# Kernel tuning notes

Measured on AMD Instinct MI355X. Metric: run time of the kernel, lower is better.

## Reference

```python
import jax, jax.numpy as jnp
import numpy as np

N_NODES = 100000
N_EDGES = 1600000
D_IN, D_H, D_OUT = 128, 128, 64


def gcn_conv(x, src, dst, W, b, n_nodes):
    """PyG GCNConv (eval): x' = D^{-1/2} (A+I) D^{-1/2} X W + b.
    src/dst already include self-loops."""
    h = x @ W  # [N, d_out] -- transform first (fewer FLOPs when d_out <= d_in)
    deg = jax.ops.segment_sum(jnp.ones_like(dst, dtype=h.dtype), dst, num_segments=n_nodes)
    dinv = jnp.where(deg > 0, jax.lax.rsqrt(deg), 0.0)
    norm = dinv[src] * dinv[dst]  # [E]
    msg = h[src] * norm[:, None]  # gather + scale
    out = jax.ops.segment_sum(msg, dst, num_segments=n_nodes)  # scatter-add
    return out + b


def setup_inputs() -> dict:
    key = jax.random.key(0)
    k = jax.random.split(key, 8)
    x = jax.random.normal(k[0], (N_NODES, D_IN), dtype=jnp.float32)
    edge_index = jax.random.randint(k[1], (2, N_EDGES), 0, N_NODES, dtype=jnp.int32)
    s = 0.1
    W1 = jax.random.normal(k[2], (D_IN, D_H), dtype=jnp.float32) * s
    b1 = jnp.zeros((D_H,), dtype=jnp.float32)
    W2 = jax.random.normal(k[3], (D_H, D_H), dtype=jnp.float32) * s
    b2 = jnp.zeros((D_H,), dtype=jnp.float32)
    W3 = jax.random.normal(k[4], (D_H, D_OUT), dtype=jnp.float32) * s
    b3 = jnp.zeros((D_OUT,), dtype=jnp.float32)
    return {"x": x, "edge_index": edge_index, "W1": W1, "b1": b1,
            "W2": W2, "b2": b2, "W3": W3, "b3": b3}


def reference(x, edge_index, W1, b1, W2, b2, W3, b3):
    n = x.shape[0]
    # add self-loops once (shared by all layers)
    loops = jnp.arange(n, dtype=edge_index.dtype)
    src = jnp.concatenate([edge_index[0], loops])
    dst = jnp.concatenate([edge_index[1], loops])
    h = gcn_conv(x, src, dst, W1, b1, n)
    h = jax.nn.relu(h)  # dropout = identity in eval mode
    h = gcn_conv(h, src, dst, W2, b2, n)
    h = jax.nn.relu(h)
    out = gcn_conv(h, src, dst, W3, b3, n)
    return out
```

## Files before the change

### kernel.cpp

```cpp
#include <hip/hip_runtime.h>
#include <hip/hip_fp16.h>

#define N_NODES 100000
#define N_EDGES 1600000
#define NBUCKET 196
#define CAP     8960
#define EPB     6250

typedef _Float16 half8 __attribute__((ext_vector_type(8)));
typedef float float4v __attribute__((ext_vector_type(4)));

__device__ __forceinline__ void fmix_lo(float& a, unsigned int w, float one) {
    asm("v_fma_mix_f32 %0, %1, %2, %0 op_sel:[0,0,0] op_sel_hi:[1,0,0]"
        : "+v"(a) : "v"(w), "v"(one));
}
__device__ __forceinline__ void fmix_hi(float& a, unsigned int w, float one) {
    asm("v_fma_mix_f32 %0, %1, %2, %0 op_sel:[1,0,0] op_sel_hi:[1,0,0]"
        : "+v"(a) : "v"(w), "v"(one));
}

__launch_bounds__(256)
__global__ void k_part_wswz(const int* __restrict__ src, const int* __restrict__ dst,
                            int* __restrict__ bcur, int* __restrict__ ebuf, int E,
                            const float* __restrict__ W1, const float* __restrict__ W2,
                            const float* __restrict__ W3, _Float16* __restrict__ wz1,
                            _Float16* __restrict__ wz2, _Float16* __restrict__ wz3) {
    if (blockIdx.x >= 256) {
        int t = (blockIdx.x - 256) * 256 + threadIdx.x;
        const float* W; _Float16* wsz; int BN;
        if (t < 2048)      { W = W1; wsz = wz1; BN = 128; }
        else if (t < 4096) { W = W2; wsz = wz2; BN = 128; t -= 2048; }
        else if (t < 5120) { W = W3; wsz = wz3; BN = 64;  t -= 4096; }
        else return;
        const int l = t & 63;
        const int kblk = (t >> 6) & 3;
        const int nt = t >> 8;
        const int krow = kblk * 32 + ((l >> 4) << 3);
        const int col = nt * 16 + (l & 15);
        _Float16 v[8];
#pragma unroll
        for (int j = 0; j < 8; ++j) v[j] = (_Float16)W[(krow + j) * BN + col];
        *(uint4*)&wsz[t << 3] = *(uint4*)v;
        return;
    }
    __shared__ int hist[200];
    __shared__ int basebkt[200];
    const int tid = threadIdx.x;
    if (tid < 200) hist[tid] = 0;
    __syncthreads();
    const int e0 = blockIdx.x * EPB, e1 = min(e0 + EPB, E);
    for (int e = e0 + tid; e < e1; e += 256) atomicAdd(&hist[dst[e] >> 9], 1);
    __syncthreads();
    if (tid < NBUCKET) {
        int h = hist[tid];
        basebkt[tid] = tid * CAP + (h ? atomicAdd(&bcur[tid], h) : 0);
    }
    __syncthreads();
    if (tid < 200) hist[tid] = 0;
    __syncthreads();
    for (int e = e0 + tid; e < e1; e += 256) {
        int d = dst[e];
        int bk = d >> 9;
        int o = atomicAdd(&hist[bk], 1);
        ebuf[basebkt[bk] + o] = (src[e] << 9) | (d & 511);
    }
}

__launch_bounds__(256)
__global__ void k_bsort(const int* __restrict__ ebuf, const int* __restrict__ bcur,
                        int* __restrict__ adj, int* __restrict__ stv,
                        int* __restrict__ deg, float* __restrict__ dinv, int N) {
    __shared__ int cnt[512];
    __shared__ int offs[512];
    const int b = blockIdx.x;
    const int tid = threadIdx.x;
    const int base = b * CAP;
    const int n_b = min(bcur[b], CAP);
    const int node0 = b << 9;
    cnt[tid] = 0; cnt[tid + 256] = 0;
    __syncthreads();
    for (int i = tid; i < n_b; i += 256)
        atomicAdd(&cnt[ebuf[base + i] & 511], 1);
    __syncthreads();
    if (tid < 64) {
        int v[8], tot = 0;
#pragma unroll
        for (int j = 0; j < 8; ++j) { int t = cnt[tid * 8 + j]; v[j] = tot; tot += t; }
        int inc = tot;
#pragma unroll
        for (int d = 1; d < 64; d <<= 1) {
            int u = __shfl_up(inc, d, 64);
            if (tid >= d) inc += u;
        }
        const int excl = inc - tot;
#pragma unroll
        for (int j = 0; j < 8; ++j) offs[tid * 8 + j] = excl + v[j];
    }
    __syncthreads();
#pragma unroll
    for (int h = 0; h < 2; ++h) {
        int local = tid + h * 256;
        int node = node0 + local;
        if (node < N) {
            stv[node] = base + offs[local];
            deg[node] = cnt[local];
            dinv[node] = rsqrtf((float)(cnt[local] + 1));
        }
    }
    __syncthreads();
    for (int i = tid; i < n_b; i += 256) {
        int pk = ebuf[base + i];
        int pos = atomicAdd(&offs[pk & 511], 1);
        adj[base + pos] = pk >> 9;
    }
}

template <int BN, bool AFP16>
__launch_bounds__(256, 4)
__global__ void k_gemm_mfma(const void* __restrict__ Xv, const _Float16* __restrict__ wsz,
                            const float* __restrict__ dinv, __half* __restrict__ out, int N) {
    constexpr int NT = BN / 16;
    constexpr int PAD = 8;
    __shared__ __align__(16) _Float16 smem[BN * 128];

    const int tid = threadIdx.x;
    for (int i = tid; i < BN * 16; i += 256)
        *(uint4*)&smem[i << 3] = *(const uint4*)&wsz[i << 3];

    const int w = tid >> 6;
    const int lane = tid & 63;
    const int q = lane >> 4;
    const int m = lane & 15;
    const int row0 = blockIdx.x * 64;
    const int arow = row0 + w * 16 + m;
    const int arowc = arow < N ? arow : N - 1;

    float4v acc[NT];
#pragma unroll
    for (int nt = 0; nt < NT; ++nt) acc[nt] = (float4v){0.f, 0.f, 0.f, 0.f};

    __syncthreads();

#pragma unroll
    for (int kblk = 0; kblk < 4; ++kblk) {
        half8 af;
        if constexpr (AFP16) {
            const _Float16* A = (const _Float16*)Xv + (size_t)arowc * 128 + (q << 3);
            af = *(const half8*)(A + kblk * 32);
        } else {
            const float* A = (const float*)Xv + (size_t)arowc * 128 + (q << 3);
            float4 a0 = *(const float4*)(A + kblk * 32);
            float4 a1 = *(const float4*)(A + kblk * 32 + 4);
            af[0] = (_Float16)a0.x; af[1] = (_Float16)a0.y;
            af[2] = (_Float16)a0.z; af[3] = (_Float16)a0.w;
            af[4] = (_Float16)a1.x; af[5] = (_Float16)a1.y;
            af[6] = (_Float16)a1.z; af[7] = (_Float16)a1.w;
        }
#pragma unroll
        for (int nt = 0; nt < NT; ++nt) {
            half8 bf = *(const half8*)&smem[(((nt << 2) + kblk) << 9) + (lane << 3)];
            acc[nt] = __builtin_amdgcn_mfma_f32_16x16x32_f16(af, bf, acc[nt], 0, 0, 0);
        }
    }

    float s[4];
#pragma unroll
    for (int r = 0; r < 4; ++r) {
        int rr = row0 + w * 16 + q * 4 + r;
        s[r] = dinv[rr < N ? rr : N - 1];
    }
    __syncthreads();
    _Float16* eb = smem;
#pragma unroll
    for (int nt = 0; nt < NT; ++nt)
#pragma unroll
        for (int r = 0; r < 4; ++r)
            eb[(w * 16 + q * 4 + r) * (BN + PAD) + nt * 16 + m] = (_Float16)(acc[nt][r] * s[r]);
    __syncthreads();
    constexpr int CPR = BN / 8;
    for (int i = tid; i < 64 * CPR; i += 256) {
        int row = i / CPR;
        int cf = (i % CPR) * 8;
        if (row0 + row < N)
            *(uint4*)&out[(size_t)(row0 + row) * BN + cf] = *(uint4*)&eb[row * (BN + PAD) + cf];
    }
}

template <bool RELU>
__launch_bounds__(256)
__global__ void k_agg128(const __half* __restrict__ tp, const int* __restrict__ adj,
                         const int* __restrict__ startv, const int* __restrict__ deg,
                         const float* __restrict__ dinv, const float* __restrict__ bias,
                         _Float16* __restrict__ out, int N) {
    const int n0 = (blockIdx.x << 3) + ((threadIdx.x >> 6) << 1);
    const int lane = threadIdx.x & 63;
    if (n0 >= N) return;
    const bool has1 = (n0 + 1) < N;
    const int n1 = has1 ? n0 + 1 : n0;
    const int s0 = startv[n0], s1 = startv[n1];
    const int c0 = deg[n0];
    const int c1 = has1 ? deg[n1] : 0;
    const float one = 1.0f;
    const int g = lane >> 4;
    const int sl = lane & 15;
    const uint4* rowb = (const uint4*)tp;

    float a0[8] = {0.f, 0.f, 0.f, 0.f, 0.f, 0.f, 0.f, 0.f};
    float a1[8] = {0.f, 0.f, 0.f, 0.f, 0.f, 0.f, 0.f, 0.f};
    auto addrow = [&](float* acc, uint4 v) {
        fmix_lo(acc[0], v.x, one); fmix_hi(acc[1], v.x, one);
        fmix_lo(acc[2], v.y, one); fmix_hi(acc[3], v.y, one);
        fmix_lo(acc[4], v.z, one); fmix_hi(acc[5], v.z, one);
        fmix_lo(acc[6], v.w, one); fmix_hi(acc[7], v.w, one);
    };

    {
        uint4 r0 = rowb[(size_t)n0 * 16 + sl];
        uint4 r1 = rowb[(size_t)n1 * 16 + sl];
        if (g == 0) { addrow(a0, r0); if (has1) addrow(a1, r1); }
    }

    int e = 0;
    const int mc = min(c0, c1);
    for (; e + 16 <= mc; e += 16) {
        int j0[4], j1[4];
#pragma unroll
        for (int u = 0; u < 4; ++u) { j0[u] = adj[s0 + e + 4 * u + g]; j1[u] = adj[s1 + e + 4 * u + g]; }
        uint4 v0[4], v1[4];
#pragma unroll
        for (int u = 0; u < 4; ++u) { v0[u] = rowb[(size_t)j0[u] * 16 + sl]; v1[u] = rowb[(size_t)j1[u] * 16 + sl]; }
#pragma unroll
        for (int u = 0; u < 4; ++u) { addrow(a0, v0[u]); addrow(a1, v1[u]); }
    }

    auto finish = [&](float* acc, int s, int cnt, int eS) {
        int ee = eS;
        for (; ee + 16 <= cnt; ee += 16) {
            int j[4];
#pragma unroll
            for (int u = 0; u < 4; ++u) j[u] = adj[s + ee + 4 * u + g];
            uint4 v[4];
#pragma unroll
            for (int u = 0; u < 4; ++u) v[u] = rowb[(size_t)j[u] * 16 + sl];
#pragma unroll
            for (int u = 0; u < 4; ++u) addrow(acc, v[u]);
        }
        if (ee + 8 <= cnt) {
            int j[2];
#pragma unroll
            for (int u = 0; u < 2; ++u) j[u] = adj[s + ee + 4 * u + g];
            uint4 v[2];
#pragma unroll
            for (int u = 0; u < 2; ++u) v[u] = rowb[(size_t)j[u] * 16 + sl];
#pragma unroll
            for (int u = 0; u < 2; ++u) addrow(acc, v[u]);
            ee += 8;
        }
        if (ee + 4 <= cnt) {
            addrow(acc, rowb[(size_t)adj[s + ee + g] * 16 + sl]);
            ee += 4;
        }
        if (ee + g < cnt)
            addrow(acc, rowb[(size_t)adj[s + ee + g] * 16 + sl]);
    };
    finish(a0, s0, c0, e);
    if (has1) finish(a1, s1, c1, e);

#pragma unroll
    for (int i = 0; i < 8; ++i) {
        a0[i] += __shfl_xor(a0[i], 32);
        a0[i] += __shfl_xor(a0[i], 16);
        a1[i] += __shfl_xor(a1[i], 32);
        a1[i] += __shfl_xor(a1[i], 16);
    }
    if (g == 0) {
        float4 b0 = *(const float4*)&bias[sl * 8];
        float4 b1 = *(const float4*)&bias[sl * 8 + 4];
        const float di0 = dinv[n0];
        float o[8];
        o[0] = di0 * a0[0] + b0.x; o[1] = di0 * a0[1] + b0.y;
        o[2] = di0 * a0[2] + b0.z; o[3] = di0 * a0[3] + b0.w;
        o[4] = di0 * a0[4] + b1.x; o[5] = di0 * a0[5] + b1.y;
        o[6] = di0 * a0[6] + b1.z; o[7] = di0 * a0[7] + b1.w;
        if (RELU)
#pragma unroll
            for (int i = 0; i < 8; ++i) o[i] = fmaxf(o[i], 0.f);
        __half2 ov[4];
#pragma unroll
        for (int i = 0; i < 4; ++i) ov[i] = __floats2half2_rn(o[2 * i], o[2 * i + 1]);
        *(uint4*)&out[(size_t)n0 * 128 + sl * 8] = *(uint4*)ov;
        if (has1) {
            const float di1 = dinv[n1];
            o[0] = di1 * a1[0] + b0.x; o[1] = di1 * a1[1] + b0.y;
            o[2] = di1 * a1[2] + b0.z; o[3] = di1 * a1[3] + b0.w;
            o[4] = di1 * a1[4] + b1.x; o[5] = di1 * a1[5] + b1.y;
            o[6] = di1 * a1[6] + b1.z; o[7] = di1 * a1[7] + b1.w;
            if (RELU)
#pragma unroll
                for (int i = 0; i < 8; ++i) o[i] = fmaxf(o[i], 0.f);
#pragma unroll
            for (int i = 0; i < 4; ++i) ov[i] = __floats2half2_rn(o[2 * i], o[2 * i + 1]);
            *(uint4*)&out[(size_t)n1 * 128 + sl * 8] = *(uint4*)ov;
        }
    }
}

__launch_bounds__(256)
__global__ void k_agg64(const __half* __restrict__ tp, const int* __restrict__ adj,
                        const int* __restrict__ startv, const int* __restrict__ deg,
                        const float* __restrict__ dinv, const float* __restrict__ bias,
                        float* __restrict__ out, int N) {
    const int n0 = (blockIdx.x << 3) + ((threadIdx.x >> 6) << 1);
    const int lane = threadIdx.x & 63;
    if (n0 >= N) return;
    const bool has1 = (n0 + 1) < N;
    const int n1 = has1 ? n0 + 1 : n0;
    const int s0 = startv[n0], s1 = startv[n1];
    const int c0 = deg[n0];
    const int c1 = has1 ? deg[n1] : 0;
    const float one = 1.0f;
    const int g = lane >> 4;
    const int sl = lane & 15;
    const uint2* rowb = (const uint2*)tp;

    float a0[4] = {0.f, 0.f, 0.f, 0.f};
    float a1[4] = {0.f, 0.f, 0.f, 0.f};
    auto addrow = [&](float* acc, uint2 v) {
        fmix_lo(acc[0], v.x, one); fmix_hi(acc[1], v.x, one);
        fmix_lo(acc[2], v.y, one); fmix_hi(acc[3], v.y, one);
    };
    {
        uint2 r0 = rowb[(size_t)n0 * 16 + sl];
        uint2 r1 = rowb[(size_t)n1 * 16 + sl];
        if (g == 0) { addrow(a0, r0); if (has1) addrow(a1, r1); }
    }

    int e = 0;
    const int mc = min(c0, c1);
    for (; e + 16 <= mc; e += 16) {
        int j0[4], j1[4];
#pragma unroll
        for (int u = 0; u < 4; ++u) { j0[u] = adj[s0 + e + 4 * u + g]; j1[u] = adj[s1 + e + 4 * u + g]; }
        uint2 v0[4], v1[4];
#pragma unroll
        for (int u = 0; u < 4; ++u) { v0[u] = rowb[(size_t)j0[u] * 16 + sl]; v1[u] = rowb[(size_t)j1[u] * 16 + sl]; }
#pragma unroll
        for (int u = 0; u < 4; ++u) { addrow(a0, v0[u]); addrow(a1, v1[u]); }
    }

    auto finish = [&](float* acc, int s, int cnt, int eS) {
        int ee = eS;
        for (; ee + 16 <= cnt; ee += 16) {
            int j[4];
#pragma unroll
            for (int u = 0; u < 4; ++u) j[u] = adj[s + ee + 4 * u + g];
            uint2 v[4];
#pragma unroll
            for (int u = 0; u < 4; ++u) v[u] = rowb[(size_t)j[u] * 16 + sl];
#pragma unroll
            for (int u = 0; u < 4; ++u) addrow(acc, v[u]);
        }
        if (ee + 8 <= cnt) {
            int j[2];
#pragma unroll
            for (int u = 0; u < 2; ++u) j[u] = adj[s + ee + 4 * u + g];
            uint2 v[2];
#pragma unroll
            for (int u = 0; u < 2; ++u) v[u] = rowb[(size_t)j[u] * 16 + sl];
#pragma unroll
            for (int u = 0; u < 2; ++u) addrow(acc, v[u]);
            ee += 8;
        }
        if (ee + 4 <= cnt) {
            addrow(acc, rowb[(size_t)adj[s + ee + g] * 16 + sl]);
            ee += 4;
        }
        if (ee + g < cnt)
            addrow(acc, rowb[(size_t)adj[s + ee + g] * 16 + sl]);
    };
    finish(a0, s0, c0, e);
    if (has1) finish(a1, s1, c1, e);

#pragma unroll
    for (int i = 0; i < 4; ++i) {
        a0[i] += __shfl_xor(a0[i], 32);
        a0[i] += __shfl_xor(a0[i], 16);
        a1[i] += __shfl_xor(a1[i], 32);
        a1[i] += __shfl_xor(a1[i], 16);
    }
    if (g == 0) {
        float4 bb = *(const float4*)&bias[sl * 4];
        const float di0 = dinv[n0];
        float4 o;
        o.x = di0 * a0[0] + bb.x; o.y = di0 * a0[1] + bb.y;
        o.z = di0 * a0[2] + bb.z; o.w = di0 * a0[3] + bb.w;
        *(float4*)&out[(size_t)n0 * 64 + sl * 4] = o;
        if (has1) {
            const float di1 = dinv[n1];
            o.x = di1 * a1[0] + bb.x; o.y = di1 * a1[1] + bb.y;
            o.z = di1 * a1[2] + bb.z; o.w = di1 * a1[3] + bb.w;
            *(float4*)&out[(size_t)n1 * 64 + sl * 4] = o;
        }
    }
}

extern "C" void kernel_launch(void* const* d_in, const int* in_sizes, int n_in,
                              void* d_out, int out_size, void* d_ws, size_t ws_size,
                              hipStream_t stream) {
    const float* x  = (const float*)d_in[0];
    const int*   ei = (const int*)d_in[1];
    const float* W1 = (const float*)d_in[2];
    const float* b1 = (const float*)d_in[3];
    const float* W2 = (const float*)d_in[4];
    const float* b2 = (const float*)d_in[5];
    const float* W3 = (const float*)d_in[6];
    const float* b3 = (const float*)d_in[7];
    float* out = (float*)d_out;
    const int* src = ei;
    const int* dst = ei + N_EDGES;

    char* p = (char*)d_ws;
    __half* tp      = (__half*)p;    p += (size_t)N_NODES * 128 * 2;
    _Float16* hbuf  = (_Float16*)p;  p += (size_t)N_NODES * 128 * 2;
    int*   deg  = (int*)p;    p += (size_t)N_NODES * 4;
    float* dinv = (float*)p;  p += (size_t)N_NODES * 4;
    int*   stv  = (int*)p;    p += (size_t)N_NODES * 4;
    int*   bCur = (int*)p;    p += 1024;
    int*   adj  = (int*)p;    p += (size_t)NBUCKET * CAP * 4 + 16384;
    _Float16* wz1 = (_Float16*)p; p += 16384 * 2;
    _Float16* wz2 = (_Float16*)p; p += 16384 * 2;
    _Float16* wz3 = (_Float16*)p; p += 8192 * 2;
    size_t need = (size_t)(p - (char*)d_ws);
    if (ws_size < need) return;

    int* ebuf = (int*)tp;

    hipMemsetAsync(bCur, 0, 1024, stream);
    k_part_wswz<<<276, 256, 0, stream>>>(src, dst, bCur, ebuf, N_EDGES,
                                         W1, W2, W3, wz1, wz2, wz3);
    k_bsort<<<NBUCKET, 256, 0, stream>>>(ebuf, bCur, adj, stv, deg, dinv, N_NODES);

    const int gb = (N_NODES + 63) / 64;
    const int ab = (N_NODES + 7) / 8;
    k_gemm_mfma<128, false><<<gb, 256, 0, stream>>>(x, wz1, dinv, tp, N_NODES);
    k_agg128<true><<<ab, 256, 0, stream>>>(tp, adj, stv, deg, dinv, b1, hbuf, N_NODES);
    k_gemm_mfma<128, true><<<gb, 256, 0, stream>>>(hbuf, wz2, dinv, tp, N_NODES);
    k_agg128<true><<<ab, 256, 0, stream>>>(tp, adj, stv, deg, dinv, b2, hbuf, N_NODES);
    k_gemm_mfma<64, true><<<gb, 256, 0, stream>>>(hbuf, wz3, dinv, tp, N_NODES);
    k_agg64<<<ab, 256, 0, stream>>>(tp, adj, stv, deg, dinv, b3, out, N_NODES);
}
```

Measured before the change: 356.4 us.

## Split aggregation feature columns across XCDs so each XCD caches one slice

```diff
diff --git a/kernel.cpp b/kernel.cpp
--- a/kernel.cpp
+++ b/kernel.cpp
@@ -192,7 +192,11 @@
                          const int* __restrict__ startv, const int* __restrict__ deg,
                          const float* __restrict__ dinv, const float* __restrict__ bias,
                          _Float16* __restrict__ out, int N) {
-    const int n0 = (blockIdx.x << 3) + ((threadIdx.x >> 6) << 1);
+    const int b = blockIdx.x;
+    const int xcd = b & 7;
+    const int sc = xcd >> 1;
+    const int bis = ((b >> 3) << 1) | (xcd & 1);
+    const int n0 = (bis << 3) + ((threadIdx.x >> 6) << 1);
     const int lane = threadIdx.x & 63;
     if (n0 >= N) return;
     const bool has1 = (n0 + 1) < N;
@@ -203,20 +207,18 @@
     const float one = 1.0f;
     const int g = lane >> 4;
     const int sl = lane & 15;
-    const uint4* rowb = (const uint4*)tp;
-
-    float a0[8] = {0.f, 0.f, 0.f, 0.f, 0.f, 0.f, 0.f, 0.f};
-    float a1[8] = {0.f, 0.f, 0.f, 0.f, 0.f, 0.f, 0.f, 0.f};
-    auto addrow = [&](float* acc, uint4 v) {
-        fmix_lo(acc[0], v.x, one); fmix_hi(acc[1], v.x, one);
-        fmix_lo(acc[2], v.y, one); fmix_hi(acc[3], v.y, one);
-        fmix_lo(acc[4], v.z, one); fmix_hi(acc[5], v.z, one);
-        fmix_lo(acc[6], v.w, one); fmix_hi(acc[7], v.w, one);
+    const unsigned* rowu = (const unsigned*)tp;
+    const int co = sc * 16 + sl;
+
+    float a0[2] = {0.f, 0.f};
+    float a1[2] = {0.f, 0.f};
+    auto addrow = [&](float* acc, unsigned v) {
+        fmix_lo(acc[0], v, one); fmix_hi(acc[1], v, one);
     };
 
     {
-        uint4 r0 = rowb[(size_t)n0 * 16 + sl];
-        uint4 r1 = rowb[(size_t)n1 * 16 + sl];
+        unsigned r0 = rowu[(size_t)n0 * 64 + co];
+        unsigned r1 = rowu[(size_t)n1 * 64 + co];
         if (g == 0) { addrow(a0, r0); if (has1) addrow(a1, r1); }
     }
 
@@ -226,9 +228,9 @@
         int j0[4], j1[4];
 #pragma unroll
         for (int u = 0; u < 4; ++u) { j0[u] = adj[s0 + e + 4 * u + g]; j1[u] = adj[s1 + e + 4 * u + g]; }
-        uint4 v0[4], v1[4];
-#pragma unroll
-        for (int u = 0; u < 4; ++u) { v0[u] = rowb[(size_t)j0[u] * 16 + sl]; v1[u] = rowb[(size_t)j1[u] * 16 + sl]; }
+        unsigned v0[4], v1[4];
+#pragma unroll
+        for (int u = 0; u < 4; ++u) { v0[u] = rowu[(size_t)j0[u] * 64 + co]; v1[u] = rowu[(size_t)j1[u] * 64 + co]; }
 #pragma unroll
         for (int u = 0; u < 4; ++u) { addrow(a0, v0[u]); addrow(a1, v1[u]); }
     }
@@ -239,9 +241,9 @@
             int j[4];
 #pragma unroll
             for (int u = 0; u < 4; ++u) j[u] = adj[s + ee + 4 * u + g];
-            uint4 v[4];
-#pragma unroll
-            for (int u = 0; u < 4; ++u) v[u] = rowb[(size_t)j[u] * 16 + sl];
+            unsigned v[4];
+#pragma unroll
+            for (int u = 0; u < 4; ++u) v[u] = rowu[(size_t)j[u] * 64 + co];
 #pragma unroll
             for (int u = 0; u < 4; ++u) addrow(acc, v[u]);
         }
@@ -249,58 +251,44 @@
             int j[2];
 #pragma unroll
             for (int u = 0; u < 2; ++u) j[u] = adj[s + ee + 4 * u + g];
-            uint4 v[2];
-#pragma unroll
-            for (int u = 0; u < 2; ++u) v[u] = rowb[(size_t)j[u] * 16 + sl];
+            unsigned v[2];
+#pragma unroll
+            for (int u = 0; u < 2; ++u) v[u] = rowu[(size_t)j[u] * 64 + co];
 #pragma unroll
             for (int u = 0; u < 2; ++u) addrow(acc, v[u]);
             ee += 8;
         }
         if (ee + 4 <= cnt) {
-            addrow(acc, rowb[(size_t)adj[s + ee + g] * 16 + sl]);
+            addrow(acc, rowu[(size_t)adj[s + ee + g] * 64 + co]);
             ee += 4;
         }
         if (ee + g < cnt)
-            addrow(acc, rowb[(size_t)adj[s + ee + g] * 16 + sl]);
+            addrow(acc, rowu[(size_t)adj[s + ee + g] * 64 + co]);
     };
     finish(a0, s0, c0, e);
     if (has1) finish(a1, s1, c1, e);
 
 #pragma unroll
-    for (int i = 0; i < 8; ++i) {
+    for (int i = 0; i < 2; ++i) {
         a0[i] += __shfl_xor(a0[i], 32);
         a0[i] += __shfl_xor(a0[i], 16);
         a1[i] += __shfl_xor(a1[i], 32);
         a1[i] += __shfl_xor(a1[i], 16);
     }
     if (g == 0) {
-        float4 b0 = *(const float4*)&bias[sl * 8];
-        float4 b1 = *(const float4*)&bias[sl * 8 + 4];
+        const float bx = bias[sc * 32 + sl * 2];
+        const float by = bias[sc * 32 + sl * 2 + 1];
         const float di0 = dinv[n0];
-        float o[8];
-        o[0] = di0 * a0[0] + b0.x; o[1] = di0 * a0[1] + b0.y;
-        o[2] = di0 * a0[2] + b0.z; o[3] = di0 * a0[3] + b0.w;
-        o[4] = di0 * a0[4] + b1.x; o[5] = di0 * a0[5] + b1.y;
-        o[6] = di0 * a0[6] + b1.z; o[7] = di0 * a0[7] + b1.w;
-        if (RELU)
-#pragma unroll
-            for (int i = 0; i < 8; ++i) o[i] = fmaxf(o[i], 0.f);
-        __half2 ov[4];
-#pragma unroll
-        for (int i = 0; i < 4; ++i) ov[i] = __floats2half2_rn(o[2 * i], o[2 * i + 1]);
-        *(uint4*)&out[(size_t)n0 * 128 + sl * 8] = *(uint4*)ov;
+        float ox = di0 * a0[0] + bx, oy = di0 * a0[1] + by;
+        if (RELU) { ox = fmaxf(ox, 0.f); oy = fmaxf(oy, 0.f); }
+        __half2 ov = __floats2half2_rn(ox, oy);
+        *(unsigned*)&out[(size_t)n0 * 128 + sc * 32 + sl * 2] = *(unsigned*)&ov;
         if (has1) {
             const float di1 = dinv[n1];
-            o[0] = di1 * a1[0] + b0.x; o[1] = di1 * a1[1] + b0.y;
-            o[2] = di1 * a1[2] + b0.z; o[3] = di1 * a1[3] + b0.w;
-            o[4] = di1 * a1[4] + b1.x; o[5] = di1 * a1[5] + b1.y;
-            o[6] = di1 * a1[6] + b1.z; o[7] = di1 * a1[7] + b1.w;
-            if (RELU)
-#pragma unroll
-                for (int i = 0; i < 8; ++i) o[i] = fmaxf(o[i], 0.f);
-#pragma unroll
-            for (int i = 0; i < 4; ++i) ov[i] = __floats2half2_rn(o[2 * i], o[2 * i + 1]);
-            *(uint4*)&out[(size_t)n1 * 128 + sl * 8] = *(uint4*)ov;
+            ox = di1 * a1[0] + bx; oy = di1 * a1[1] + by;
+            if (RELU) { ox = fmaxf(ox, 0.f); oy = fmaxf(oy, 0.f); }
+            ov = __floats2half2_rn(ox, oy);
+            *(unsigned*)&out[(size_t)n1 * 128 + sc * 32 + sl * 2] = *(unsigned*)&ov;
         }
     }
 }
@@ -310,7 +298,11 @@
                         const int* __restrict__ startv, const int* __restrict__ deg,
                         const float* __restrict__ dinv, const float* __restrict__ bias,
                         float* __restrict__ out, int N) {
-    const int n0 = (blockIdx.x << 3) + ((threadIdx.x >> 6) << 1);
+    const int b = blockIdx.x;
+    const int xcd = b & 7;
+    const int sc = xcd >> 2;
+    const int bis = ((b >> 3) << 2) | (xcd & 3);
+    const int n0 = (bis << 3) + ((threadIdx.x >> 6) << 1);
     const int lane = threadIdx.x & 63;
     if (n0 >= N) return;
     const bool has1 = (n0 + 1) < N;
@@ -321,17 +313,17 @@
     const float one = 1.0f;
     const int g = lane >> 4;
     const int sl = lane & 15;
-    const uint2* rowb = (const uint2*)tp;
-
-    float a0[4] = {0.f, 0.f, 0.f, 0.f};
-    float a1[4] = {0.f, 0.f, 0.f, 0.f};
-    auto addrow = [&](float* acc, uint2 v) {
-        fmix_lo(acc[0], v.x, one); fmix_hi(acc[1], v.x, one);
-        fmix_lo(acc[2], v.y, one); fmix_hi(acc[3], v.y, one);
+    const unsigned* rowu = (const unsigned*)tp;
+    const int co = sc * 16 + sl;
+
+    float a0[2] = {0.f, 0.f};
+    float a1[2] = {0.f, 0.f};
+    auto addrow = [&](float* acc, unsigned v) {
+        fmix_lo(acc[0], v, one); fmix_hi(acc[1], v, one);
     };
     {
-        uint2 r0 = rowb[(size_t)n0 * 16 + sl];
-        uint2 r1 = rowb[(size_t)n1 * 16 + sl];
+        unsigned r0 = rowu[(size_t)n0 * 32 + co];
+        unsigned r1 = rowu[(size_t)n1 * 32 + co];
         if (g == 0) { addrow(a0, r0); if (has1) addrow(a1, r1); }
     }
 
@@ -341,9 +333,9 @@
         int j0[4], j1[4];
 #pragma unroll
         for (int u = 0; u < 4; ++u) { j0[u] = adj[s0 + e + 4 * u + g]; j1[u] = adj[s1 + e + 4 * u + g]; }
-        uint2 v0[4], v1[4];
-#pragma unroll
-        for (int u = 0; u < 4; ++u) { v0[u] = rowb[(size_t)j0[u] * 16 + sl]; v1[u] = rowb[(size_t)j1[u] * 16 + sl]; }
+        unsigned v0[4], v1[4];
+#pragma unroll
+        for (int u = 0; u < 4; ++u) { v0[u] = rowu[(size_t)j0[u] * 32 + co]; v1[u] = rowu[(size_t)j1[u] * 32 + co]; }
 #pragma unroll
         for (int u = 0; u < 4; ++u) { addrow(a0, v0[u]); addrow(a1, v1[u]); }
     }
@@ -354,9 +346,9 @@
             int j[4];
 #pragma unroll
             for (int u = 0; u < 4; ++u) j[u] = adj[s + ee + 4 * u + g];
-            uint2 v[4];
-#pragma unroll
-            for (int u = 0; u < 4; ++u) v[u] = rowb[(size_t)j[u] * 16 + sl];
+            unsigned v[4];
+#pragma unroll
+            for (int u = 0; u < 4; ++u) v[u] = rowu[(size_t)j[u] * 32 + co];
 #pragma unroll
             for (int u = 0; u < 4; ++u) addrow(acc, v[u]);
         }
@@ -364,42 +356,41 @@
             int j[2];
 #pragma unroll
             for (int u = 0; u < 2; ++u) j[u] = adj[s + ee + 4 * u + g];
-            uint2 v[2];
-#pragma unroll
-            for (int u = 0; u < 2; ++u) v[u] = rowb[(size_t)j[u] * 16 + sl];
+            unsigned v[2];
+#pragma unroll
+            for (int u = 0; u < 2; ++u) v[u] = rowu[(size_t)j[u] * 32 + co];
 #pragma unroll
             for (int u = 0; u < 2; ++u) addrow(acc, v[u]);
             ee += 8;
         }
         if (ee + 4 <= cnt) {
-            addrow(acc, rowb[(size_t)adj[s + ee + g] * 16 + sl]);
+            addrow(acc, rowu[(size_t)adj[s + ee + g] * 32 + co]);
             ee += 4;
         }
         if (ee + g < cnt)
-            addrow(acc, rowb[(size_t)adj[s + ee + g] * 16 + sl]);
+            addrow(acc, rowu[(size_t)adj[s + ee + g] * 32 + co]);
     };
     finish(a0, s0, c0, e);
     if (has1) finish(a1, s1, c1, e);
 
 #pragma unroll
-    for (int i = 0; i < 4; ++i) {
+    for (int i = 0; i < 2; ++i) {
         a0[i] += __shfl_xor(a0[i], 32);
         a0[i] += __shfl_xor(a0[i], 16);
         a1[i] += __shfl_xor(a1[i], 32);
         a1[i] += __shfl_xor(a1[i], 16);
     }
     if (g == 0) {
-        float4 bb = *(const float4*)&bias[sl * 4];
+        const float bx = bias[sc * 32 + sl * 2];
+        const float by = bias[sc * 32 + sl * 2 + 1];
         const float di0 = dinv[n0];
-        float4 o;
-        o.x = di0 * a0[0] + bb.x; o.y = di0 * a0[1] + bb.y;
-        o.z = di0 * a0[2] + bb.z; o.w = di0 * a0[3] + bb.w;
-        *(float4*)&out[(size_t)n0 * 64 + sl * 4] = o;
+        float2 o;
+        o.x = di0 * a0[0] + bx; o.y = di0 * a0[1] + by;
+        *(float2*)&out[(size_t)n0 * 64 + sc * 32 + sl * 2] = o;
         if (has1) {
             const float di1 = dinv[n1];
-            o.x = di1 * a1[0] + bb.x; o.y = di1 * a1[1] + bb.y;
-            o.z = di1 * a1[2] + bb.z; o.w = di1 * a1[3] + bb.w;
-            *(float4*)&out[(size_t)n1 * 64 + sl * 4] = o;
+            o.x = di1 * a1[0] + bx; o.y = di1 * a1[1] + by;
+            *(float2*)&out[(size_t)n1 * 64 + sc * 32 + sl * 2] = o;
         }
     }
 }
@@ -441,11 +432,12 @@
     k_bsort<<<NBUCKET, 256, 0, stream>>>(ebuf, bCur, adj, stv, deg, dinv, N_NODES);
 
     const int gb = (N_NODES + 63) / 64;
-    const int ab = (N_NODES + 7) / 8;
+    const int ab128 = 12500 * 4;
+    const int ab64  = 12500 * 2;
     k_gemm_mfma<128, false><<<gb, 256, 0, stream>>>(x, wz1, dinv, tp, N_NODES);
-    k_agg128<true><<<ab, 256, 0, stream>>>(tp, adj, stv, deg, dinv, b1, hbuf, N_NODES);
+    k_agg128<true><<<ab128, 256, 0, stream>>>(tp, adj, stv, deg, dinv, b1, hbuf, N_NODES);
     k_gemm_mfma<128, true><<<gb, 256, 0, stream>>>(hbuf, wz2, dinv, tp, N_NODES);
-    k_agg128<true><<<ab, 256, 0, stream>>>(tp, adj, stv, deg, dinv, b2, hbuf, N_NODES);
+    k_agg128<true><<<ab128, 256, 0, stream>>>(tp, adj, stv, deg, dinv, b2, hbuf, N_NODES);
     k_gemm_mfma<64, true><<<gb, 256, 0, stream>>>(hbuf, wz3, dinv, tp, N_NODES);
-    k_agg64<<<ab, 256, 0, stream>>>(tp, adj, stv, deg, dinv, b3, out, N_NODES);
-}
+    k_agg64<<<ab64, 256, 0, stream>>>(tp, adj, stv, deg, dinv, b3, out, N_NODES);
+}
```

Result: slower. 531.3 us (+49.1%).

## Fuse all GCN stages into one persistent cooperative kernel with grid syncs

Applied to the files above, without the earlier changes.

```diff
diff --git a/kernel.cpp b/kernel.cpp
--- a/kernel.cpp
+++ b/kernel.cpp
@@ -1,11 +1,16 @@
 #include <hip/hip_runtime.h>
 #include <hip/hip_fp16.h>
+#include <hip/hip_cooperative_groups.h>
+
+namespace cg = cooperative_groups;
 
 #define N_NODES 100000
 #define N_EDGES 1600000
 #define NBUCKET 196
 #define CAP     8960
 #define EPB     6250
+#define VB_GEMM ((N_NODES + 63) / 64)
+#define VB_AGG  ((N_NODES + 7) / 8)
 
 typedef _Float16 half8 __attribute__((ext_vector_type(8)));
 typedef float float4v __attribute__((ext_vector_type(4)));
@@ -19,36 +24,33 @@
         : "+v"(a) : "v"(w), "v"(one));
 }
 
-__launch_bounds__(256)
-__global__ void k_part_wswz(const int* __restrict__ src, const int* __restrict__ dst,
-                            int* __restrict__ bcur, int* __restrict__ ebuf, int E,
-                            const float* __restrict__ W1, const float* __restrict__ W2,
-                            const float* __restrict__ W3, _Float16* __restrict__ wz1,
-                            _Float16* __restrict__ wz2, _Float16* __restrict__ wz3) {
-    if (blockIdx.x >= 256) {
-        int t = (blockIdx.x - 256) * 256 + threadIdx.x;
-        const float* W; _Float16* wsz; int BN;
-        if (t < 2048)      { W = W1; wsz = wz1; BN = 128; }
-        else if (t < 4096) { W = W2; wsz = wz2; BN = 128; t -= 2048; }
-        else if (t < 5120) { W = W3; wsz = wz3; BN = 64;  t -= 4096; }
-        else return;
-        const int l = t & 63;
-        const int kblk = (t >> 6) & 3;
-        const int nt = t >> 8;
-        const int krow = kblk * 32 + ((l >> 4) << 3);
-        const int col = nt * 16 + (l & 15);
-        _Float16 v[8];
-#pragma unroll
-        for (int j = 0; j < 8; ++j) v[j] = (_Float16)W[(krow + j) * BN + col];
-        *(uint4*)&wsz[t << 3] = *(uint4*)v;
-        return;
-    }
-    __shared__ int hist[200];
-    __shared__ int basebkt[200];
-    const int tid = threadIdx.x;
+
+__device__ __forceinline__ void wswz_one(int t, const float* __restrict__ W1,
+                                         const float* __restrict__ W2, const float* __restrict__ W3,
+                                         _Float16* __restrict__ wz1, _Float16* __restrict__ wz2,
+                                         _Float16* __restrict__ wz3) {
+    const float* W; _Float16* wsz; int BN;
+    if (t < 2048)      { W = W1; wsz = wz1; BN = 128; }
+    else if (t < 4096) { W = W2; wsz = wz2; BN = 128; t -= 2048; }
+    else               { W = W3; wsz = wz3; BN = 64;  t -= 4096; }
+    const int l = t & 63;
+    const int kblk = (t >> 6) & 3;
+    const int nt = t >> 8;
+    const int krow = kblk * 32 + ((l >> 4) << 3);
+    const int col = nt * 16 + (l & 15);
+    _Float16 v[8];
+#pragma unroll
+    for (int j = 0; j < 8; ++j) v[j] = (_Float16)W[(krow + j) * BN + col];
+    *(uint4*)&wsz[t << 3] = *(uint4*)v;
+}
+
+__device__ __forceinline__ void d_part(int vb, int tid, int* hist, int* basebkt,
+                                       const int* __restrict__ src, const int* __restrict__ dst,
+                                       int* __restrict__ bcur, int* __restrict__ ebuf, int E) {
+    __syncthreads();
     if (tid < 200) hist[tid] = 0;
     __syncthreads();
-    const int e0 = blockIdx.x * EPB, e1 = min(e0 + EPB, E);
+    const int e0 = vb * EPB, e1 = min(e0 + EPB, E);
     for (int e = e0 + tid; e < e1; e += 256) atomicAdd(&hist[dst[e] >> 9], 1);
     __syncthreads();
     if (tid < NBUCKET) {
@@ -66,17 +68,14 @@
     }
 }
 
-__launch_bounds__(256)
-__global__ void k_bsort(const int* __restrict__ ebuf, const int* __restrict__ bcur,
-                        int* __restrict__ adj, int* __restrict__ stv,
-                        int* __restrict__ deg, float* __restrict__ dinv, int N) {
-    __shared__ int cnt[512];
-    __shared__ int offs[512];
-    const int b = blockIdx.x;
-    const int tid = threadIdx.x;
-    const int base = b * CAP;
-    const int n_b = min(bcur[b], CAP);
-    const int node0 = b << 9;
+__device__ __forceinline__ void d_bsort(int vb, int tid, int* cnt, int* offs,
+                                        const int* __restrict__ ebuf, const int* __restrict__ bcur,
+                                        int* __restrict__ adj, int* __restrict__ stv,
+                                        int* __restrict__ deg, float* __restrict__ dinv, int N) {
+    __syncthreads();
+    const int base = vb * CAP;
+    const int n_b = min(bcur[vb], CAP);
+    const int node0 = vb << 9;
     cnt[tid] = 0; cnt[tid + 256] = 0;
     __syncthreads();
     for (int i = tid; i < n_b; i += 256)
@@ -116,14 +115,12 @@
 }
 
 template <int BN, bool AFP16>
-__launch_bounds__(256, 4)
-__global__ void k_gemm_mfma(const void* __restrict__ Xv, const _Float16* __restrict__ wsz,
-                            const float* __restrict__ dinv, __half* __restrict__ out, int N) {
+__device__ __forceinline__ void d_gemm(int vb, int tid, _Float16* smem,
+                                       const void* __restrict__ Xv, const _Float16* __restrict__ wsz,
+                                       const float* __restrict__ dinv, __half* __restrict__ out, int N) {
     constexpr int NT = BN / 16;
     constexpr int PAD = 8;
-    __shared__ __align__(16) _Float16 smem[BN * 128];
-
-    const int tid = threadIdx.x;
+    __syncthreads();
     for (int i = tid; i < BN * 16; i += 256)
         *(uint4*)&smem[i << 3] = *(const uint4*)&wsz[i << 3];
 
@@ -131,7 +128,7 @@
     const int lane = tid & 63;
     const int q = lane >> 4;
     const int m = lane & 15;
-    const int row0 = blockIdx.x * 64;
+    const int row0 = vb * 64;
     const int arow = row0 + w * 16 + m;
     const int arowc = arow < N ? arow : N - 1;
 
@@ -187,13 +184,13 @@
 }
 
 template <bool RELU>
-__launch_bounds__(256)
-__global__ void k_agg128(const __half* __restrict__ tp, const int* __restrict__ adj,
-                         const int* __restrict__ startv, const int* __restrict__ deg,
-                         const float* __restrict__ dinv, const float* __restrict__ bias,
-                         _Float16* __restrict__ out, int N) {
-    const int n0 = (blockIdx.x << 3) + ((threadIdx.x >> 6) << 1);
-    const int lane = threadIdx.x & 63;
+__device__ __forceinline__ void d_agg128(int vb, int tid,
+                                         const __half* __restrict__ tp, const int* __restrict__ adj,
+                                         const int* __restrict__ startv, const int* __restrict__ deg,
+                                         const float* __restrict__ dinv, const float* __restrict__ bias,
+                                         _Float16* __restrict__ out, int N) {
+    const int n0 = (vb << 3) + ((tid >> 6) << 1);
+    const int lane = tid & 63;
     if (n0 >= N) return;
     const bool has1 = (n0 + 1) < N;
     const int n1 = has1 ? n0 + 1 : n0;
@@ -305,13 +302,13 @@
     }
 }
 
-__launch_bounds__(256)
-__global__ void k_agg64(const __half* __restrict__ tp, const int* __restrict__ adj,
-                        const int* __restrict__ startv, const int* __restrict__ deg,
-                        const float* __restrict__ dinv, const float* __restrict__ bias,
-                        float* __restrict__ out, int N) {
-    const int n0 = (blockIdx.x << 3) + ((threadIdx.x >> 6) << 1);
-    const int lane = threadIdx.x & 63;
+__device__ __forceinline__ void d_agg64(int vb, int tid,
+                                        const __half* __restrict__ tp, const int* __restrict__ adj,
+                                        const int* __restrict__ startv, const int* __restrict__ deg,
+                                        const float* __restrict__ dinv, const float* __restrict__ bias,
+                                        float* __restrict__ out, int N) {
+    const int n0 = (vb << 3) + ((tid >> 6) << 1);
+    const int lane = tid & 63;
     if (n0 >= N) return;
     const bool has1 = (n0 + 1) < N;
     const int n1 = has1 ? n0 + 1 : n0;
@@ -402,6 +399,100 @@
             *(float4*)&out[(size_t)n1 * 64 + sl * 4] = o;
         }
     }
+}
+
+__global__ void __launch_bounds__(256, 4)
+k_mega(const float* x, const int* src, const int* dst,
+       const float* W1, const float* W2, const float* W3,
+       const float* b1, const float* b2, const float* b3,
+       float* out, __half* tp, _Float16* hbuf,
+       int* deg, float* dinv, int* stv, int* bcur, int* adj,
+       _Float16* wz1, _Float16* wz2, _Float16* wz3) {
+    __shared__ __align__(16) _Float16 smem[128 * 128];
+    int* ilds = (int*)smem;
+    cg::grid_group gg = cg::this_grid();
+    const int tid = threadIdx.x;
+    const int nb = gridDim.x;
+    int* ebuf = (int*)tp;
+
+    {
+        const int gid = blockIdx.x * 256 + tid;
+        for (int t = gid; t < 5120; t += nb * 256)
+            wswz_one(t, W1, W2, W3, wz1, wz2, wz3);
+        for (int i = gid; i < 256; i += nb * 256) bcur[i] = 0;
+    }
+    gg.sync();
+    for (int vb = blockIdx.x; vb < 256; vb += nb)
+        d_part(vb, tid, ilds, ilds + 200, src, dst, bcur, ebuf, N_EDGES);
+    gg.sync();
+    for (int vb = blockIdx.x; vb < NBUCKET; vb += nb)
+        d_bsort(vb, tid, ilds, ilds + 512, ebuf, bcur, adj, stv, deg, dinv, N_NODES);
+    gg.sync();
+    for (int vb = blockIdx.x; vb < VB_GEMM; vb += nb)
+        d_gemm<128, false>(vb, tid, smem, x, wz1, dinv, tp, N_NODES);
+    gg.sync();
+    for (int vb = blockIdx.x; vb < VB_AGG; vb += nb)
+        d_agg128<true>(vb, tid, tp, adj, stv, deg, dinv, b1, hbuf, N_NODES);
+    gg.sync();
+    for (int vb = blockIdx.x; vb < VB_GEMM; vb += nb)
+        d_gemm<128, true>(vb, tid, smem, hbuf, wz2, dinv, tp, N_NODES);
+    gg.sync();
+    for (int vb = blockIdx.x; vb < VB_AGG; vb += nb)
+        d_agg128<true>(vb, tid, tp, adj, stv, deg, dinv, b2, hbuf, N_NODES);
+    gg.sync();
+    for (int vb = blockIdx.x; vb < VB_GEMM; vb += nb)
+        d_gemm<64, true>(vb, tid, smem, hbuf, wz3, dinv, tp, N_NODES);
+    gg.sync();
+    for (int vb = blockIdx.x; vb < VB_AGG; vb += nb)
+        d_agg64(vb, tid, (const __half*)tp, adj, stv, deg, dinv, b3, out, N_NODES);
+}
+
+__launch_bounds__(256)
+__global__ void k_part_wswz(const int* __restrict__ src, const int* __restrict__ dst,
+                            int* __restrict__ bcur, int* __restrict__ ebuf, int E,
+                            const float* __restrict__ W1, const float* __restrict__ W2,
+                            const float* __restrict__ W3, _Float16* __restrict__ wz1,
+                            _Float16* __restrict__ wz2, _Float16* __restrict__ wz3) {
+    __shared__ int hb[400];
+    if (blockIdx.x >= 256) {
+        int t = (blockIdx.x - 256) * 256 + threadIdx.x;
+        if (t < 5120) wswz_one(t, W1, W2, W3, wz1, wz2, wz3);
+        return;
+    }
+    d_part(blockIdx.x, threadIdx.x, hb, hb + 200, src, dst, bcur, ebuf, E);
+}
+
+__launch_bounds__(256)
+__global__ void k_bsort(const int* __restrict__ ebuf, const int* __restrict__ bcur,
+                        int* __restrict__ adj, int* __restrict__ stv,
+                        int* __restrict__ deg, float* __restrict__ dinv, int N) {
+    __shared__ int cb[1024];
+    d_bsort(blockIdx.x, threadIdx.x, cb, cb + 512, ebuf, bcur, adj, stv, deg, dinv, N);
+}
+
+template <int BN, bool AFP16>
+__launch_bounds__(256, 4)
+__global__ void k_gemm_mfma(const void* __restrict__ Xv, const _Float16* __restrict__ wsz,
+                            const float* __restrict__ dinv, __half* __restrict__ out, int N) {
+    __shared__ __align__(16) _Float16 smem[BN * 128];
+    d_gemm<BN, AFP16>(blockIdx.x, threadIdx.x, smem, Xv, wsz, dinv, out, N);
+}
+
+template <bool RELU>
+__launch_bounds__(256)
+__global__ void k_agg128(const __half* __restrict__ tp, const int* __restrict__ adj,
+                         const int* __restrict__ startv, const int* __restrict__ deg,
+                         const float* __restrict__ dinv, const float* __restrict__ bias,
+                         _Float16* __restrict__ out, int N) {
+    d_agg128<RELU>(blockIdx.x, threadIdx.x, tp, adj, startv, deg, dinv, bias, out, N);
+}
+
+__launch_bounds__(256)
+__global__ void k_agg64(const __half* __restrict__ tp, const int* __restrict__ adj,
+                        const int* __restrict__ startv, const int* __restrict__ deg,
+                        const float* __restrict__ dinv, const float* __restrict__ bias,
+                        float* __restrict__ out, int N) {
+    d_agg64(blockIdx.x, threadIdx.x, tp, adj, startv, deg, dinv, bias, out, N);
 }
 
 extern "C" void kernel_launch(void* const* d_in, const int* in_sizes, int n_in,
@@ -435,13 +526,30 @@
 
     int* ebuf = (int*)tp;
 
+    int maxb = 0;
+    hipError_t oe = hipOccupancyMaxActiveBlocksPerMultiprocessor(&maxb, k_mega, 256, 0);
+    int nblocks = (oe == hipSuccess && maxb > 0) ? min(1024, maxb * 256) : 0;
+    hipError_t cerr = hipErrorUnknown;
+    if (nblocks > 0) {
+        void* kargs[] = {(void*)&x, (void*)&src, (void*)&dst,
+                         (void*)&W1, (void*)&W2, (void*)&W3,
+                         (void*)&b1, (void*)&b2, (void*)&b3,
+                         (void*)&out, (void*)&tp, (void*)&hbuf,
+                         (void*)&deg, (void*)&dinv, (void*)&stv,
+                         (void*)&bCur, (void*)&adj,
+                         (void*)&wz1, (void*)&wz2, (void*)&wz3};
+        cerr = hipLaunchCooperativeKernel((const void*)k_mega, dim3(nblocks), dim3(256),
+                                          kargs, 0, stream);
+    }
+    if (cerr == hipSuccess) return;
+
     hipMemsetAsync(bCur, 0, 1024, stream);
     k_part_wswz<<<276, 256, 0, stream>>>(src, dst, bCur, ebuf, N_EDGES,
                                          W1, W2, W3, wz1, wz2, wz3);
     k_bsort<<<NBUCKET, 256, 0, stream>>>(ebuf, bCur, adj, stv, deg, dinv, N_NODES);
 
-    const int gb = (N_NODES + 63) / 64;
-    const int ab = (N_NODES + 7) / 8;
+    const int gb = VB_GEMM;
+    const int ab = VB_AGG;
     k_gemm_mfma<128, false><<<gb, 256, 0, stream>>>(x, wz1, dinv, tp, N_NODES);
     k_agg128<true><<<ab, 256, 0, stream>>>(tp, adj, stv, deg, dinv, b1, hbuf, N_NODES);
     k_gemm_mfma<128, true><<<gb, 256, 0, stream>>>(hbuf, wz2, dinv, tp, N_NODES);
```

Result: slower. 1.014 ms (+184.5%).

## Fuse aggregation with next layer's GEMM via shared-memory MFMA tile

Applied to the files above, without the earlier changes.

```diff
diff --git a/kernel.cpp b/kernel.cpp
--- a/kernel.cpp
+++ b/kernel.cpp
@@ -186,20 +186,25 @@
     }
 }
 
-template <bool RELU>
-__launch_bounds__(256)
-__global__ void k_agg128(const __half* __restrict__ tp, const int* __restrict__ adj,
+template <int BN>
+__launch_bounds__(512)
+__global__ void k_aggemm(const __half* __restrict__ tp, const int* __restrict__ adj,
                          const int* __restrict__ startv, const int* __restrict__ deg,
                          const float* __restrict__ dinv, const float* __restrict__ bias,
-                         _Float16* __restrict__ out, int N) {
-    const int n0 = (blockIdx.x << 3) + ((threadIdx.x >> 6) << 1);
-    const int lane = threadIdx.x & 63;
-    if (n0 >= N) return;
-    const bool has1 = (n0 + 1) < N;
-    const int n1 = has1 ? n0 + 1 : n0;
-    const int s0 = startv[n0], s1 = startv[n1];
-    const int c0 = deg[n0];
-    const int c1 = has1 ? deg[n1] : 0;
+                         const _Float16* __restrict__ wsz, __half* __restrict__ outtp, int N) {
+    __shared__ __align__(16) _Float16 hl[16][136];
+    const int tid = threadIdx.x;
+    const int w = tid >> 6;
+    const int lane = tid & 63;
+    const int blk0 = blockIdx.x << 4;
+    const int n0 = blk0 + (w << 1);
+    const bool v0 = n0 < N;
+    const bool v1 = (n0 + 1) < N;
+    const int nn0 = v0 ? n0 : 0;
+    const int nn1 = v1 ? n0 + 1 : nn0;
+    const int s0 = v0 ? startv[nn0] : 0, s1 = v1 ? startv[nn1] : 0;
+    const int c0 = v0 ? deg[nn0] : 0;
+    const int c1 = v1 ? deg[nn1] : 0;
     const float one = 1.0f;
     const int g = lane >> 4;
     const int sl = lane & 15;
@@ -214,10 +219,10 @@
         fmix_lo(acc[6], v.w, one); fmix_hi(acc[7], v.w, one);
     };
 
-    {
-        uint4 r0 = rowb[(size_t)n0 * 16 + sl];
-        uint4 r1 = rowb[(size_t)n1 * 16 + sl];
-        if (g == 0) { addrow(a0, r0); if (has1) addrow(a1, r1); }
+    if (v0) {
+        uint4 r0 = rowb[(size_t)nn0 * 16 + sl];
+        uint4 r1 = rowb[(size_t)nn1 * 16 + sl];
+        if (g == 0) { addrow(a0, r0); if (v1) addrow(a1, r1); }
     }
 
     int e = 0;
@@ -226,11 +231,11 @@
         int j0[4], j1[4];
 #pragma unroll
         for (int u = 0; u < 4; ++u) { j0[u] = adj[s0 + e + 4 * u + g]; j1[u] = adj[s1 + e + 4 * u + g]; }
-        uint4 v0[4], v1[4];
-#pragma unroll
-        for (int u = 0; u < 4; ++u) { v0[u] = rowb[(size_t)j0[u] * 16 + sl]; v1[u] = rowb[(size_t)j1[u] * 16 + sl]; }
-#pragma unroll
-        for (int u = 0; u < 4; ++u) { addrow(a0, v0[u]); addrow(a1, v1[u]); }
+        uint4 v0v[4], v1v[4];
+#pragma unroll
+        for (int u = 0; u < 4; ++u) { v0v[u] = rowb[(size_t)j0[u] * 16 + sl]; v1v[u] = rowb[(size_t)j1[u] * 16 + sl]; }
+#pragma unroll
+        for (int u = 0; u < 4; ++u) { addrow(a0, v0v[u]); addrow(a1, v1v[u]); }
     }
 
     auto finish = [&](float* acc, int s, int cnt, int eS) {
@@ -264,7 +269,7 @@
             addrow(acc, rowb[(size_t)adj[s + ee + g] * 16 + sl]);
     };
     finish(a0, s0, c0, e);
-    if (has1) finish(a1, s1, c1, e);
+    if (v1) finish(a1, s1, c1, e);
 
 #pragma unroll
     for (int i = 0; i < 8; ++i) {
@@ -273,34 +278,48 @@
         a1[i] += __shfl_xor(a1[i], 32);
         a1[i] += __shfl_xor(a1[i], 16);
     }
-    if (g == 0) {
+    if (g == 0 && v0) {
         float4 b0 = *(const float4*)&bias[sl * 8];
         float4 b1 = *(const float4*)&bias[sl * 8 + 4];
-        const float di0 = dinv[n0];
+        const float di0 = dinv[nn0];
         float o[8];
-        o[0] = di0 * a0[0] + b0.x; o[1] = di0 * a0[1] + b0.y;
-        o[2] = di0 * a0[2] + b0.z; o[3] = di0 * a0[3] + b0.w;
-        o[4] = di0 * a0[4] + b1.x; o[5] = di0 * a0[5] + b1.y;
-        o[6] = di0 * a0[6] + b1.z; o[7] = di0 * a0[7] + b1.w;
-        if (RELU)
-#pragma unroll
-            for (int i = 0; i < 8; ++i) o[i] = fmaxf(o[i], 0.f);
+        o[0] = fmaxf(di0 * a0[0] + b0.x, 0.f); o[1] = fmaxf(di0 * a0[1] + b0.y, 0.f);
+        o[2] = fmaxf(di0 * a0[2] + b0.z, 0.f); o[3] = fmaxf(di0 * a0[3] + b0.w, 0.f);
+        o[4] = fmaxf(di0 * a0[4] + b1.x, 0.f); o[5] = fmaxf(di0 * a0[5] + b1.y, 0.f);
+        o[6] = fmaxf(di0 * a0[6] + b1.z, 0.f); o[7] = fmaxf(di0 * a0[7] + b1.w, 0.f);
         __half2 ov[4];
 #pragma unroll
         for (int i = 0; i < 4; ++i) ov[i] = __floats2half2_rn(o[2 * i], o[2 * i + 1]);
-        *(uint4*)&out[(size_t)n0 * 128 + sl * 8] = *(uint4*)ov;
-        if (has1) {
-            const float di1 = dinv[n1];
-            o[0] = di1 * a1[0] + b0.x; o[1] = di1 * a1[1] + b0.y;
-            o[2] = di1 * a1[2] + b0.z; o[3] = di1 * a1[3] + b0.w;
-            o[4] = di1 * a1[4] + b1.x; o[5] = di1 * a1[5] + b1.y;
-            o[6] = di1 * a1[6] + b1.z; o[7] = di1 * a1[7] + b1.w;
-            if (RELU)
-#pragma unroll
-                for (int i = 0; i < 8; ++i) o[i] = fmaxf(o[i], 0.f);
+        *(uint4*)&hl[w * 2][sl * 8] = *(uint4*)ov;
+        if (v1) {
+            const float di1 = dinv[nn1];
+            o[0] = fmaxf(di1 * a1[0] + b0.x, 0.f); o[1] = fmaxf(di1 * a1[1] + b0.y, 0.f);
+            o[2] = fmaxf(di1 * a1[2] + b0.z, 0.f); o[3] = fmaxf(di1 * a1[3] + b0.w, 0.f);
+            o[4] = fmaxf(di1 * a1[4] + b1.x, 0.f); o[5] = fmaxf(di1 * a1[5] + b1.y, 0.f);
+            o[6] = fmaxf(di1 * a1[6] + b1.z, 0.f); o[7] = fmaxf(di1 * a1[7] + b1.w, 0.f);
 #pragma unroll
             for (int i = 0; i < 4; ++i) ov[i] = __floats2half2_rn(o[2 * i], o[2 * i + 1]);
-            *(uint4*)&out[(size_t)n1 * 128 + sl * 8] = *(uint4*)ov;
+            *(uint4*)&hl[w * 2 + 1][sl * 8] = *(uint4*)ov;
+        }
+    }
+    __syncthreads();
+
+    if (w < BN / 16) {
+        const int q = lane >> 4;
+        const int m = lane & 15;
+        float4v acc = (float4v){0.f, 0.f, 0.f, 0.f};
+#pragma unroll
+        for (int kblk = 0; kblk < 4; ++kblk) {
+            half8 af = *(const half8*)&hl[m][(q << 3) + kblk * 32];
+            half8 bf = *(const half8*)&wsz[(((w << 2) + kblk) << 9) + (lane << 3)];
+            acc = __builtin_amdgcn_mfma_f32_16x16x32_f16(af, bf, acc, 0, 0, 0);
+        }
+#pragma unroll
+        for (int r = 0; r < 4; ++r) {
+            const int row = q * 4 + r;
+            const int node = blk0 + row;
+            if (node < N)
+                outtp[(size_t)node * BN + w * 16 + m] = __float2half(acc[r] * dinv[node]);
         }
     }
 }
@@ -420,8 +439,8 @@
     const int* dst = ei + N_EDGES;
 
     char* p = (char*)d_ws;
-    __half* tp      = (__half*)p;    p += (size_t)N_NODES * 128 * 2;
-    _Float16* hbuf  = (_Float16*)p;  p += (size_t)N_NODES * 128 * 2;
+    __half* tpA     = (__half*)p;    p += (size_t)N_NODES * 128 * 2;
+    __half* tpB     = (__half*)p;    p += (size_t)N_NODES * 128 * 2;
     int*   deg  = (int*)p;    p += (size_t)N_NODES * 4;
     float* dinv = (float*)p;  p += (size_t)N_NODES * 4;
     int*   stv  = (int*)p;    p += (size_t)N_NODES * 4;
@@ -433,7 +452,7 @@
     size_t need = (size_t)(p - (char*)d_ws);
     if (ws_size < need) return;
 
-    int* ebuf = (int*)tp;
+    int* ebuf = (int*)tpA;
 
     hipMemsetAsync(bCur, 0, 1024, stream);
     k_part_wswz<<<276, 256, 0, stream>>>(src, dst, bCur, ebuf, N_EDGES,
@@ -441,11 +460,10 @@
     k_bsort<<<NBUCKET, 256, 0, stream>>>(ebuf, bCur, adj, stv, deg, dinv, N_NODES);
 
     const int gb = (N_NODES + 63) / 64;
+    const int fb = (N_NODES + 15) / 16;
     const int ab = (N_NODES + 7) / 8;
-    k_gemm_mfma<128, false><<<gb, 256, 0, stream>>>(x, wz1, dinv, tp, N_NODES);
-    k_agg128<true><<<ab, 256, 0, stream>>>(tp, adj, stv, deg, dinv, b1, hbuf, N_NODES);
-    k_gemm_mfma<128, true><<<gb, 256, 0, stream>>>(hbuf, wz2, dinv, tp, N_NODES);
-    k_agg128<true><<<ab, 256, 0, stream>>>(tp, adj, stv, deg, dinv, b2, hbuf, N_NODES);
-    k_gemm_mfma<64, true><<<gb, 256, 0, stream>>>(hbuf, wz3, dinv, tp, N_NODES);
-    k_agg64<<<ab, 256, 0, stream>>>(tp, adj, stv, deg, dinv, b3, out, N_NODES);
-}
+    k_gemm_mfma<128, false><<<gb, 256, 0, stream>>>(x, wz1, dinv, tpA, N_NODES);
+    k_aggemm<128><<<fb, 512, 0, stream>>>(tpA, adj, stv, deg, dinv, b1, wz2, tpB, N_NODES);
+    k_aggemm<64><<<fb, 512, 0, stream>>>(tpB, adj, stv, deg, dinv, b2, wz3, tpA, N_NODES);
+    k_agg64<<<ab, 256, 0, stream>>>(tpA, adj, stv, deg, dinv, b3, out, N_NODES);
+}
```

After: 354.0 us. About the same (-0.7%).
